# Optimization experiments

Measured on AMD Instinct MI355X. Metric: run time of the kernel, lower is better.

The kernel has to match this reference:

```python
import jax, jax.numpy as jnp
import numpy as np


def setup_inputs() -> dict:
    key = jax.random.key(0)
    ks = jax.random.split(key, 10)
    B, S, D = 16, 2048, 256
    return {
        "x": jax.random.normal(ks[0], (B, S, D), dtype=jnp.float32),
        "noise": jax.random.normal(ks[1], (B, S, D), dtype=jnp.float32),
        "alpha1": jax.random.normal(ks[2], (D,), dtype=jnp.float32),
        "alpha2": jax.random.normal(ks[3], (D,), dtype=jnp.float32),
        "W_ttt": jax.random.normal(ks[4], (D, D), dtype=jnp.float32),
        "W_proj": jax.random.normal(ks[5], (D, D), dtype=jnp.float32),
        "ff_alpha": jax.random.normal(ks[6], (D,), dtype=jnp.float32),
        "ff_beta": jax.random.normal(ks[7], (D,), dtype=jnp.float32),
        "ff_gamma": jax.random.normal(ks[8], (1,), dtype=jnp.float32),
        "ff_eta": jax.random.normal(ks[9], (1,), dtype=jnp.float32),
    }


def _ttt(W, m, noise):
    # m, noise: [B, S, D]; sequential SGD on W over the sequence axis.
    B, S, D = m.shape
    scale = 2.0 / (B * D)  # d(mse)/d(pred) factor

    def step(W, inp):
        state, eps = inp                      # [B, D] each
        train = state + eps
        diff = train @ W.T - state            # pred - label, [B, D]
        grad = scale * (diff.T @ train)       # dL/dW, [D, D]
        Wn = W - 0.01 * grad
        return Wn, state @ Wn.T               # readout with updated W

    _, outs = jax.lax.scan(step, W, (jnp.swapaxes(m, 0, 1), jnp.swapaxes(noise, 0, 1)))
    return jnp.swapaxes(outs, 0, 1)           # [B, S, D]


def reference(x, noise, alpha1, alpha2, W_ttt, W_proj, ff_alpha, ff_beta, ff_gamma, ff_eta):
    # memory path: VecDyT norm then TTT (readouts are detached in torch)
    m = jnp.tanh(alpha1 * x)
    mem = jax.lax.stop_gradient(_ttt(W_ttt, m, noise))

    # feedforward path: VecDyT norm then FFUnit
    v = jnp.tanh(alpha2 * x)
    u = ff_gamma * jax.nn.gelu(ff_alpha * v, approximate=False) + ff_eta * jnp.sin(ff_beta * v)
    g = u * (v @ W_proj.T)

    return mem + g
```

## Files before the change

kernel.cpp:

```cpp
#include <hip/hip_runtime.h>

typedef unsigned short u16;
typedef unsigned int u32;
typedef __attribute__((ext_vector_type(8))) short bf16x8;
typedef __attribute__((ext_vector_type(4))) float f32x4;

#define SB 16
#define SS 2048
#define SD 256
#define CC 16
#define NCH (SS / CC)
#define KAPPA 4.8828125e-6f
#define RP 24
#define SLOT 65536

__device__ __forceinline__ u16 f2bf(float f) {
  u32 u = __float_as_uint(f);
  u = (u + 0x7FFFu + ((u >> 16) & 1u)) >> 16;
  return (u16)u;
}
__device__ __forceinline__ float bf2f(u16 u) { return __uint_as_float((u32)u << 16); }

__device__ __forceinline__ bf16x8 ldfrag(const u16* p) {
  union { uint4 u; bf16x8 f; } cv;
  cv.u = *(const uint4*)p;
  return cv.f;
}
__device__ __forceinline__ bf16x8 asfrag(uint4 q) {
  union { uint4 u; bf16x8 f; } cv;
  cv.u = q;
  return cv.f;
}
__device__ __forceinline__ f32x4 mfma16(bf16x8 a, bf16x8 b, f32x4 c) {
  return __builtin_amdgcn_mfma_f32_16x16x32_bf16(a, b, c, 0, 0, 0);
}

__global__ __launch_bounds__(256) void prep_kernel(
    const float* __restrict__ x, const float* __restrict__ noise,
    const float* __restrict__ a1,
    u16* __restrict__ train, u16* __restrict__ state, u16* __restrict__ trainT) {
  size_t i4 = (size_t)blockIdx.x * 256 + threadIdx.x;
  size_t base = i4 * 4;
  int d = (int)(base & 255);
  int t = (int)((base >> 8) & 2047);
  int b = (int)(base >> 19);
  float4 xv = *(const float4*)(x + base);
  float4 nv = *(const float4*)(noise + base);
  float4 av = *(const float4*)(a1 + d);
  float m0 = tanhf(av.x * xv.x);
  float m1 = tanhf(av.y * xv.y);
  float m2 = tanhf(av.z * xv.z);
  float m3 = tanhf(av.w * xv.w);
  size_t dst = ((size_t)t * SB + b) * SD + d;
  ushort4 tr, st;
  tr.x = f2bf(m0 + nv.x); tr.y = f2bf(m1 + nv.y);
  tr.z = f2bf(m2 + nv.z); tr.w = f2bf(m3 + nv.w);
  st.x = f2bf(m0); st.y = f2bf(m1); st.z = f2bf(m2); st.w = f2bf(m3);
  *(ushort4*)(train + dst) = tr;
  *(ushort4*)(state + dst) = st;
  size_t tb = ((size_t)t * SD + d) * SB + b;
  trainT[tb + 0 * SB] = tr.x;
  trainT[tb + 1 * SB] = tr.y;
  trainT[tb + 2 * SB] = tr.z;
  trainT[tb + 3 * SB] = tr.w;
}

__global__ __launch_bounds__(256) void gram2ff_kernel(
    const u16* __restrict__ tr, const u16* __restrict__ st,
    u16* __restrict__ AG, u16* __restrict__ LbG,
    const float* __restrict__ x, const float* __restrict__ a2,
    const float* __restrict__ Wp, const float* __restrict__ ffa,
    const float* __restrict__ ffb, const float* __restrict__ ffg_,
    const float* __restrict__ ffe_, float* __restrict__ out) {
  __shared__ float As[32][68];
  __shared__ float Bs[32][68];
  const int tid = threadIdx.x;

  if (blockIdx.x < 2048) {
    const int cb = blockIdx.x;
    const int c = cb >> 4, t = cb & 15;
    const int lane = tid & 63, wv = tid >> 6;
    const int lr = lane & 15, lq = lane >> 4;
    const size_t Tt = (size_t)cb;
    bf16x8 trF[8], stF[8];
#pragma unroll
    for (int k = 0; k < 8; ++k) {
      trF[k] = ldfrag(tr + (Tt * 16 + lr) * 256 + k * 32 + lq * 8);
      stF[k] = ldfrag(st + (Tt * 16 + lr) * 256 + k * 32 + lq * 8);
    }
    for (int ii = 0; ii < 2; ++ii) {
      const int sp = wv + ii * 4;
      u16* dA = AG + ((size_t)cb * 8 + sp) * 512;
      u16* dL = LbG + ((size_t)cb * 8 + sp) * 512;
#pragma unroll
      for (int h = 0; h < 2; ++h) {
        const int s = 2 * sp + h;
        f32x4 accA = {0.f, 0.f, 0.f, 0.f}, accL = {0.f, 0.f, 0.f, 0.f};
        if (s <= t) {
          const u16* bsrc = tr + ((size_t)(c * 16 + s) * 16 + lr) * 256 + lq * 8;
#pragma unroll
          for (int k = 0; k < 8; ++k) {
            bf16x8 bk = ldfrag(bsrc + k * 32);
            if (s < t) accA = mfma16(trF[k], bk, accA);
            accL = mfma16(stF[k], bk, accL);
          }
        }
#pragma unroll
        for (int r = 0; r < 4; ++r) {
          int idx = (lq * 4 + r) * 32 + h * 16 + lr;
          dA[idx] = (s < t) ? f2bf(accA[r]) : (u16)0;
          dL[idx] = (s <= t) ? f2bf(accL[r]) : (u16)0;
        }
      }
    }
    return;
  }

  const int fb = blockIdx.x - 2048;
  const int gm0 = (fb >> 2) * 64;
  const int gn0 = (fb & 3) * 64;
  const int tm = tid & 15, tn = tid >> 4;
  const int lr = tid & 63;
  const int lq = tid >> 6;
  float acc[4][4];
#pragma unroll
  for (int i = 0; i < 4; i++)
#pragma unroll
    for (int j = 0; j < 4; j++) acc[i][j] = 0.f;

  for (int k0 = 0; k0 < 256; k0 += 32) {
    {
      const float* xp = x + (size_t)(gm0 + lr) * 256 + k0 + lq * 8;
      float4 v0 = *(const float4*)(xp);
      float4 v1 = *(const float4*)(xp + 4);
      const float* ap = a2 + k0 + lq * 8;
      float4 a0 = *(const float4*)(ap);
      float4 a1v = *(const float4*)(ap + 4);
      As[lq * 8 + 0][lr] = tanhf(a0.x * v0.x);
      As[lq * 8 + 1][lr] = tanhf(a0.y * v0.y);
      As[lq * 8 + 2][lr] = tanhf(a0.z * v0.z);
      As[lq * 8 + 3][lr] = tanhf(a0.w * v0.w);
      As[lq * 8 + 4][lr] = tanhf(a1v.x * v1.x);
      As[lq * 8 + 5][lr] = tanhf(a1v.y * v1.y);
      As[lq * 8 + 6][lr] = tanhf(a1v.z * v1.z);
      As[lq * 8 + 7][lr] = tanhf(a1v.w * v1.w);
      const float* wp = Wp + (size_t)(gn0 + lr) * 256 + k0 + lq * 8;
      float4 w0 = *(const float4*)(wp);
      float4 w1 = *(const float4*)(wp + 4);
      Bs[lq * 8 + 0][lr] = w0.x; Bs[lq * 8 + 1][lr] = w0.y;
      Bs[lq * 8 + 2][lr] = w0.z; Bs[lq * 8 + 3][lr] = w0.w;
      Bs[lq * 8 + 4][lr] = w1.x; Bs[lq * 8 + 5][lr] = w1.y;
      Bs[lq * 8 + 6][lr] = w1.z; Bs[lq * 8 + 7][lr] = w1.w;
    }
    __syncthreads();
#pragma unroll
    for (int k = 0; k < 32; ++k) {
      float4 av4 = *(const float4*)&As[k][tm * 4];
      float4 bv4 = *(const float4*)&Bs[k][tn * 4];
      float a[4] = {av4.x, av4.y, av4.z, av4.w};
      float b[4] = {bv4.x, bv4.y, bv4.z, bv4.w};
#pragma unroll
      for (int i = 0; i < 4; i++)
#pragma unroll
        for (int j = 0; j < 4; j++) acc[i][j] += a[i] * b[j];
    }
    __syncthreads();
  }
  const float ga = ffg_[0], et = ffe_[0];
#pragma unroll
  for (int ii = 0; ii < 4; ++ii) {
    int row = gm0 + tm * 4 + ii;
    int col = gn0 + tn * 4;
    float4 xv = *(const float4*)(x + (size_t)row * 256 + col);
    float4 fa = *(const float4*)(ffa + col);
    float4 fb4 = *(const float4*)(ffb + col);
    float4 a2v = *(const float4*)(a2 + col);
    float xs[4] = {xv.x, xv.y, xv.z, xv.w};
    float fas[4] = {fa.x, fa.y, fa.z, fa.w};
    float fbs[4] = {fb4.x, fb4.y, fb4.z, fb4.w};
    float a2s[4] = {a2v.x, a2v.y, a2v.z, a2v.w};
    float res[4];
#pragma unroll
    for (int j = 0; j < 4; ++j) {
      float v = tanhf(a2s[j] * xs[j]);
      float z = fas[j] * v;
      float gelu = 0.5f * z * (1.0f + erff(z * 0.70710678118654752f));
      float u = ga * gelu + et * sinf(fbs[j] * v);
      res[j] = u * acc[ii][j];
    }
    float4 o; o.x = res[0]; o.y = res[1]; o.z = res[2]; o.w = res[3];
    *(float4*)(out + (size_t)row * 256 + col) = o;
  }
}

__global__ __launch_bounds__(512) void phaseA_kernel(
    const u16* __restrict__ tr, const u16* __restrict__ st,
    const u16* __restrict__ trT, const u16* __restrict__ AG,
    u16* __restrict__ Dt, u16* __restrict__ Qb) {
  __shared__ u16 StT[CC][16 * RP];
  __shared__ u16 YtL[CC][16 * RP];
  __shared__ u16 ZtL[CC][16 * RP];
  const int tid = threadIdx.x;
  const int lane = tid & 63;
  const int w = tid >> 6;
  const int d1b = blockIdx.x;
  const int c = blockIdx.y;
  const int lr = lane & 15;
  const int lq = lane >> 4;

  uint4 agR[2][8];
#pragma unroll
  for (int u = 0; u < 2; ++u) {
    const u16* ag = AG + ((size_t)(c * 16 + w + 8 * u) * 8) * 512 + lr * 32 + lq * 8;
#pragma unroll
    for (int sp = 0; sp < 8; ++sp) agR[u][sp] = *(const uint4*)(ag + sp * 512);
  }
  u16 sraw[2][4];
  float xs[2][4];
#pragma unroll
  for (int u = 0; u < 2; ++u) {
    const size_t T = (size_t)c * CC + w + 8 * u;
    ushort4 pk;
#pragma unroll
    for (int r = 0; r < 4; ++r) {
      size_t idx = (T * 16 + lq * 4 + r) * 256 + d1b * 16 + lr;
      sraw[u][r] = st[idx];
      xs[u][r] = bf2f(tr[idx]);
      ((u16*)&pk)[r] = sraw[u][r];
    }
    *(ushort4*)(&StT[w + 8 * u][lr * RP + lq * 4]) = pk;
  }
  __syncthreads();

#pragma unroll
  for (int u = 0; u < 2; ++u) {
    f32x4 a1 = {0.f, 0.f, 0.f, 0.f}, a2 = {0.f, 0.f, 0.f, 0.f};
#pragma unroll
    for (int sp = 0; sp < 8; ++sp) {
      const int s0 = 2 * sp + (lq >> 1);
      bf16x8 xb = ldfrag(trT + ((size_t)(c * CC + s0) * 256 + d1b * 16 + lr) * 16 +
                         (lq & 1) * 8);
      bf16x8 sb = ldfrag(&StT[s0][lr * RP + (lq & 1) * 8]);
      a1 = mfma16(asfrag(agR[u][sp]), xb, a1);
      a2 = mfma16(asfrag(agR[u][sp]), sb, a2);
    }
    ushort4 py, pz;
#pragma unroll
    for (int r = 0; r < 4; ++r) {
      ((u16*)&py)[r] = f2bf(xs[u][r] - KAPPA * a1[r]);
      ((u16*)&pz)[r] = f2bf(bf2f(sraw[u][r]) - KAPPA * a2[r]);
    }
    *(ushort4*)(&YtL[w + 8 * u][lr * RP + lq * 4]) = py;
    *(ushort4*)(&ZtL[w + 8 * u][lr * RP + lq * 4]) = pz;
  }
  __syncthreads();

  bf16x8 yf[8], zf[8];
#pragma unroll
  for (int sp = 0; sp < 8; ++sp) {
    yf[sp] = ldfrag(&YtL[2 * sp + (lq >> 1)][lr * RP + (lq & 1) * 8]);
    zf[sp] = ldfrag(&ZtL[2 * sp + (lq >> 1)][lr * RP + (lq & 1) * 8]);
  }
  const size_t base = (size_t)c * SLOT;
#pragma unroll
  for (int u = 0; u < 2; ++u) {
    const int d2b = w + 8 * u;
    f32x4 da = {0.f, 0.f, 0.f, 0.f}, qa = {0.f, 0.f, 0.f, 0.f};
#pragma unroll
    for (int sp = 0; sp < 8; ++sp) {
      bf16x8 xb = ldfrag(trT + ((size_t)(c * CC + 2 * sp + (lq >> 1)) * 256 +
                                d2b * 16 + lr) * 16 + (lq & 1) * 8);
      da = mfma16(yf[sp], xb, da);
      qa = mfma16(zf[sp], xb, qa);
    }
#pragma unroll
    for (int r = 0; r < 4; ++r) {
      Dt[base + (size_t)(d2b * 16 + lr) * 256 + d1b * 16 + lq * 4 + r] =
          f2bf(-KAPPA * da[r]);
      Qb[base + (size_t)(d1b * 16 + lq * 4 + r) * 256 + d2b * 16 + lr] =
          f2bf(KAPPA * qa[r]);
    }
  }
}

__global__ __launch_bounds__(512) void kq_kernel(
    const u16* __restrict__ Dt, u16* __restrict__ Qb, int lev) {
  const int qn = blockIdx.x >> 4, rb = blockIdx.x & 15;
  const int half = 1 << (lev - 1);
  const int blk = qn >> (lev - 1), win = qn & (half - 1);
  const int i = blk * half * 2 + half + win;
  const int j = blk * half * 2 + half - 1;
  u16* Qi = Qb + (size_t)i * SLOT;
  const u16* Qj = Qb + (size_t)j * SLOT;
  const u16* Dti = Dt + (size_t)i * SLOT;
  const int lane = threadIdx.x & 63, w = threadIdx.x >> 6;
  const int lr = lane & 15, lq = lane >> 4;
  bf16x8 aq[8];
#pragma unroll
  for (int kb = 0; kb < 8; ++kb)
    aq[kb] = ldfrag(Qj + (size_t)(rb * 16 + lr) * 256 + kb * 32 + lq * 8);
#pragma unroll
  for (int u = 0; u < 2; ++u) {
    const int cb = w + 8 * u;
    f32x4 acc = {0.f, 0.f, 0.f, 0.f};
#pragma unroll
    for (int kb = 0; kb < 8; ++kb) {
      bf16x8 bf = ldfrag(Dti + (size_t)(cb * 16 + lr) * 256 + kb * 32 + lq * 8);
      acc = mfma16(aq[kb], bf, acc);
    }
#pragma unroll
    for (int r = 0; r < 4; ++r) {
      size_t idx = (size_t)(rb * 16 + lq * 4 + r) * 256 + cb * 16 + lr;
      float v = acc[r] + bf2f(Qj[idx]) + bf2f(Qi[idx]);
      Qi[idx] = f2bf(v);
    }
  }
}

__global__ __launch_bounds__(512) void kd_kernel(u16* __restrict__ Dt, int lev) {
  const int qn = blockIdx.x >> 4, rb = blockIdx.x & 15;
  const int half = 1 << (lev - 1);
  const int blk = qn >> (lev - 1), win = qn & (half - 1);
  const int i = blk * half * 2 + half + win;
  const int j = blk * half * 2 + half - 1;
  u16* Dti = Dt + (size_t)i * SLOT;
  const u16* Dtj = Dt + (size_t)j * SLOT;
  const int lane = threadIdx.x & 63, w = threadIdx.x >> 6;
  const int lr = lane & 15, lq = lane >> 4;
  bf16x8 ad[8];
#pragma unroll
  for (int kb = 0; kb < 8; ++kb)
    ad[kb] = ldfrag(Dti + (size_t)(rb * 16 + lr) * 256 + kb * 32 + lq * 8);
  float oldv[2][4];
#pragma unroll
  for (int u = 0; u < 2; ++u) {
    const int cb = w + 8 * u;
#pragma unroll
    for (int r = 0; r < 4; ++r) {
      size_t idx = (size_t)(rb * 16 + lq * 4 + r) * 256 + cb * 16 + lr;
      oldv[u][r] = bf2f(Dtj[idx]) + bf2f(Dti[idx]);
    }
  }
  __syncthreads();
#pragma unroll
  for (int u = 0; u < 2; ++u) {
    const int cb = w + 8 * u;
    f32x4 acc = {0.f, 0.f, 0.f, 0.f};
#pragma unroll
    for (int kb = 0; kb < 8; ++kb) {
      union { u16 s[8]; bf16x8 f; } bv;
#pragma unroll
      for (int e = 0; e < 8; ++e)
        bv.s[e] = Dtj[(size_t)(kb * 32 + lq * 8 + e) * 256 + cb * 16 + lr];
      acc = mfma16(ad[kb], bv.f, acc);
    }
#pragma unroll
    for (int r = 0; r < 4; ++r) {
      size_t idx = (size_t)(rb * 16 + lq * 4 + r) * 256 + cb * 16 + lr;
      Dti[idx] = f2bf(acc[r] + oldv[u][r]);
    }
  }
}

__global__ __launch_bounds__(512) void phaseC_kernel(
    const u16* __restrict__ tr, const u16* __restrict__ st,
    const u16* __restrict__ AG, const u16* __restrict__ LbG,
    const u16* __restrict__ Dt, const u16* __restrict__ Qb,
    const float* __restrict__ Wttt, float* __restrict__ out) {
  __shared__ u16 RpL[CC][16 * RP];
  __shared__ u16 DpL[CC][16 * RP];
  __shared__ u16 WbL[16][268];

  const int tid = threadIdx.x;
  const int lane = tid & 63;
  const int w = tid >> 6;
  const int d1b = blockIdx.x;
  const int c = blockIdx.y;
  const int lr = lane & 15;
  const int lq = lane >> 4;

  {
    bf16x8 wf[8];
#pragma unroll
    for (int kb = 0; kb < 8; ++kb) {
      const float* wp = Wttt + (size_t)(d1b * 16 + lr) * 256 + kb * 32 + lq * 8;
      float4 w0 = *(const float4*)(wp);
      float4 w1 = *(const float4*)(wp + 4);
      union { u16 s[8]; bf16x8 f; } cv;
      cv.s[0] = f2bf(w0.x); cv.s[1] = f2bf(w0.y);
      cv.s[2] = f2bf(w0.z); cv.s[3] = f2bf(w0.w);
      cv.s[4] = f2bf(w1.x); cv.s[5] = f2bf(w1.y);
      cv.s[6] = f2bf(w1.z); cv.s[7] = f2bf(w1.w);
      wf[kb] = cv.f;
    }
    const size_t ex = (size_t)(c - 1) * SLOT;
#pragma unroll
    for (int u = 0; u < 2; ++u) {
      const int cb = w + 8 * u;
      f32x4 acc = {0.f, 0.f, 0.f, 0.f};
      if (c > 0) {
#pragma unroll
        for (int kb = 0; kb < 8; ++kb) {
          bf16x8 bf = ldfrag(Dt + ex + (size_t)(cb * 16 + lr) * 256 + kb * 32 + lq * 8);
          acc = mfma16(wf[kb], bf, acc);
        }
      }
#pragma unroll
      for (int r = 0; r < 4; ++r) {
        size_t ri = (size_t)(d1b * 16 + lq * 4 + r) * 256 + cb * 16 + lr;
        float v = Wttt[ri] + acc[r];
        if (c > 0) v += bf2f(Qb[ex + (size_t)(d1b * 16 + lq * 4 + r) * 256 + cb * 16 + lr]);
        WbL[lq * 4 + r][cb * 16 + lr] = f2bf(v);
      }
    }
  }
  __syncthreads();

  uint4 agR[2][8];
#pragma unroll
  for (int u = 0; u < 2; ++u) {
    const u16* ag = AG + ((size_t)(c * 16 + w + 8 * u) * 8) * 512 + lr * 32 + lq * 8;
#pragma unroll
    for (int sp = 0; sp < 8; ++sp) agR[u][sp] = *(const uint4*)(ag + sp * 512);
  }
  uint4 trR[2][8], stR[2][8];
  float sub[2][4];
#pragma unroll
  for (int u = 0; u < 2; ++u) {
    const size_t T = (size_t)c * CC + w + 8 * u;
    const u16* trt = tr + (T * 16 + lr) * 256 + lq * 8;
    const u16* stt = st + (T * 16 + lr) * 256 + lq * 8;
#pragma unroll
    for (int k = 0; k < 8; ++k) {
      trR[u][k] = *(const uint4*)(trt + k * 32);
      stR[u][k] = *(const uint4*)(stt + k * 32);
    }
#pragma unroll
    for (int r = 0; r < 4; ++r)
      sub[u][r] = bf2f(st[(T * 16 + lq * 4 + r) * 256 + d1b * 16 + lr]);
  }

  f32x4 rhsF[2], qF[2];
#pragma unroll
  for (int u = 0; u < 2; ++u) {
    f32x4 racc = {0.f, 0.f, 0.f, 0.f}, qacc = {0.f, 0.f, 0.f, 0.f};
#pragma unroll
    for (int k = 0; k < 8; ++k) {
      bf16x8 wb = ldfrag(&WbL[lr][k * 32 + lq * 8]);
      racc = mfma16(asfrag(trR[u][k]), wb, racc);
      qacc = mfma16(asfrag(stR[u][k]), wb, qacc);
    }
#pragma unroll
    for (int r = 0; r < 4; ++r) racc[r] -= sub[u][r];
    rhsF[u] = racc; qF[u] = qacc;
    ushort4 pk;
    pk.x = f2bf(racc.x); pk.y = f2bf(racc.y);
    pk.z = f2bf(racc.z); pk.w = f2bf(racc.w);
    *(ushort4*)(&RpL[w + 8 * u][lr * RP + lq * 4]) = pk;
  }
  __syncthreads();

  uint4 lbR[2][8];
#pragma unroll
  for (int u = 0; u < 2; ++u) {
    const u16* lb = LbG + ((size_t)(c * 16 + w + 8 * u) * 8) * 512 + lr * 32 + lq * 8;
#pragma unroll
    for (int sp = 0; sp < 8; ++sp) lbR[u][sp] = *(const uint4*)(lb + sp * 512);
  }

#pragma unroll
  for (int u = 0; u < 2; ++u) {
    f32x4 acc = {0.f, 0.f, 0.f, 0.f};
#pragma unroll
    for (int sp = 0; sp < 8; ++sp) {
      bf16x8 bf = ldfrag(&RpL[2 * sp + (lq >> 1)][lr * RP + (lq & 1) * 8]);
      acc = mfma16(asfrag(agR[u][sp]), bf, acc);
    }
    ushort4 pk;
#pragma unroll
    for (int r = 0; r < 4; ++r) {
      float dv = rhsF[u][r] - KAPPA * acc[r];
      ((u16*)&pk)[r] = f2bf(-KAPPA * dv);
    }
    *(ushort4*)(&DpL[w + 8 * u][lr * RP + lq * 4]) = pk;
  }
  __syncthreads();

  float gp[2][4];
#pragma unroll
  for (int u = 0; u < 2; ++u) {
    const size_t T = (size_t)c * CC + w + 8 * u;
#pragma unroll
    for (int r = 0; r < 4; ++r)
      gp[u][r] = out[((size_t)(lq * 4 + r) * SS + T) * SD + d1b * 16 + lr];
  }
#pragma unroll
  for (int u = 0; u < 2; ++u) {
    const size_t T = (size_t)c * CC + w + 8 * u;
    f32x4 acc = qF[u];
#pragma unroll
    for (int sp = 0; sp < 8; ++sp) {
      bf16x8 bf = ldfrag(&DpL[2 * sp + (lq >> 1)][lr * RP + (lq & 1) * 8]);
      acc = mfma16(asfrag(lbR[u][sp]), bf, acc);
    }
#pragma unroll
    for (int r = 0; r < 4; ++r) {
      size_t oi = ((size_t)(lq * 4 + r) * SS + T) * SD + d1b * 16 + lr;
      out[oi] = acc[r] + gp[u][r];
    }
  }
}

extern "C" void kernel_launch(void* const* d_in, const int* in_sizes, int n_in,
                              void* d_out, int out_size, void* d_ws, size_t ws_size,
                              hipStream_t stream) {
  const float* x     = (const float*)d_in[0];
  const float* noise = (const float*)d_in[1];
  const float* a1    = (const float*)d_in[2];
  const float* a2    = (const float*)d_in[3];
  const float* Wttt  = (const float*)d_in[4];
  const float* Wproj = (const float*)d_in[5];
  const float* ffa   = (const float*)d_in[6];
  const float* ffb   = (const float*)d_in[7];
  const float* ffg   = (const float*)d_in[8];
  const float* ffe   = (const float*)d_in[9];
  float* out = (float*)d_out;

  const size_t N = (size_t)SB * SS * SD;
  u16* tr  = (u16*)d_ws;
  u16* st  = tr + N;
  u16* trT = st + N;
  u16* AG  = trT + N;
  u16* LbG = AG + N;
  u16* Dt  = LbG + N;
  u16* Qb  = Dt + N;

  prep_kernel<<<8192, 256, 0, stream>>>(x, noise, a1, tr, st, trT);
  gram2ff_kernel<<<4096, 256, 0, stream>>>(tr, st, AG, LbG,
                                           x, a2, Wproj, ffa, ffb, ffg, ffe, out);
  phaseA_kernel<<<dim3(16, 128), 512, 0, stream>>>(tr, st, trT, AG, Dt, Qb);
  for (int lev = 1; lev <= 7; ++lev) {
    kq_kernel<<<1024, 512, 0, stream>>>(Dt, Qb, lev);
    kd_kernel<<<1024, 512, 0, stream>>>(Dt, lev);
  }
  phaseC_kernel<<<dim3(16, 128), 512, 0, stream>>>(tr, st, AG, LbG, Dt, Qb,
                                                   Wttt, out);
}
```

Baseline: 873.8 us.

## Mirror D in transposed layout and precompute per-chunk start weights

Keeps a second copy of the D matrices (Db) in the transposed layout, so the kd scan kernel can load its B operand with vectorized fragment loads instead of strided scalar gathers. The scan kernel now writes both layouts. Per-chunk starting weights W+W·D+Q are computed once per chunk in a new wstart kernel and stored in bf16 in a reused trT buffer, so the 16 phaseC blocks per chunk no longer each redo that GEMM. The cost is extra global writes for the mirror and for the Wsb buffer, plus one more kernel launch.

```diff
diff --git a/kernel.cpp b/kernel.cpp
--- a/kernel.cpp
+++ b/kernel.cpp
@@ -196,7 +196,7 @@
 __global__ __launch_bounds__(512) void phaseA_kernel(
     const u16* __restrict__ tr, const u16* __restrict__ st,
     const u16* __restrict__ trT, const u16* __restrict__ AG,
-    u16* __restrict__ Dt, u16* __restrict__ Qb) {
+    u16* __restrict__ Dt, u16* __restrict__ Db, u16* __restrict__ Qb) {
   __shared__ u16 StT[CC][16 * RP];
   __shared__ u16 YtL[CC][16 * RP];
   __shared__ u16 ZtL[CC][16 * RP];
@@ -273,13 +273,16 @@
       da = mfma16(yf[sp], xb, da);
       qa = mfma16(zf[sp], xb, qa);
     }
-#pragma unroll
-    for (int r = 0; r < 4; ++r) {
-      Dt[base + (size_t)(d2b * 16 + lr) * 256 + d1b * 16 + lq * 4 + r] =
-          f2bf(-KAPPA * da[r]);
+    ushort4 dpk;
+#pragma unroll
+    for (int r = 0; r < 4; ++r) {
+      const u16 dv = f2bf(-KAPPA * da[r]);
+      ((u16*)&dpk)[r] = dv;
+      Db[base + (size_t)(d1b * 16 + lq * 4 + r) * 256 + d2b * 16 + lr] = dv;
       Qb[base + (size_t)(d1b * 16 + lq * 4 + r) * 256 + d2b * 16 + lr] =
           f2bf(KAPPA * qa[r]);
     }
+    *(ushort4*)(Dt + base + (size_t)(d2b * 16 + lr) * 256 + d1b * 16 + lq * 4) = dpk;
   }
 }
 
@@ -317,7 +320,8 @@
   }
 }
 
-__global__ __launch_bounds__(512) void kd_kernel(u16* __restrict__ Dt, int lev) {
+__global__ __launch_bounds__(512) void kdt_kernel(
+    u16* __restrict__ Dt, u16* __restrict__ Db, int lev) {
   const int qn = blockIdx.x >> 4, rb = blockIdx.x & 15;
   const int half = 1 << (lev - 1);
   const int blk = qn >> (lev - 1), win = qn & (half - 1);
@@ -325,6 +329,8 @@
   const int j = blk * half * 2 + half - 1;
   u16* Dti = Dt + (size_t)i * SLOT;
   const u16* Dtj = Dt + (size_t)j * SLOT;
+  u16* Dbi = Db + (size_t)i * SLOT;
+  const u16* Dbj = Db + (size_t)j * SLOT;
   const int lane = threadIdx.x & 63, w = threadIdx.x >> 6;
   const int lr = lane & 15, lq = lane >> 4;
   bf16x8 ad[8];
@@ -348,42 +354,45 @@
     f32x4 acc = {0.f, 0.f, 0.f, 0.f};
 #pragma unroll
     for (int kb = 0; kb < 8; ++kb) {
-      union { u16 s[8]; bf16x8 f; } bv;
-#pragma unroll
-      for (int e = 0; e < 8; ++e)
-        bv.s[e] = Dtj[(size_t)(kb * 32 + lq * 8 + e) * 256 + cb * 16 + lr];
-      acc = mfma16(ad[kb], bv.f, acc);
-    }
-#pragma unroll
-    for (int r = 0; r < 4; ++r) {
-      size_t idx = (size_t)(rb * 16 + lq * 4 + r) * 256 + cb * 16 + lr;
-      Dti[idx] = f2bf(acc[r] + oldv[u][r]);
-    }
-  }
-}
-
-__global__ __launch_bounds__(512) void phaseC_kernel(
-    const u16* __restrict__ tr, const u16* __restrict__ st,
-    const u16* __restrict__ AG, const u16* __restrict__ LbG,
-    const u16* __restrict__ Dt, const u16* __restrict__ Qb,
-    const float* __restrict__ Wttt, float* __restrict__ out) {
-  __shared__ u16 RpL[CC][16 * RP];
-  __shared__ u16 DpL[CC][16 * RP];
-  __shared__ u16 WbL[16][268];
-
+      bf16x8 bf = ldfrag(Dbj + (size_t)(cb * 16 + lr) * 256 + kb * 32 + lq * 8);
+      acc = mfma16(ad[kb], bf, acc);
+    }
+    ushort4 mir;
+#pragma unroll
+    for (int r = 0; r < 4; ++r) {
+      const u16 nv = f2bf(acc[r] + oldv[u][r]);
+      ((u16*)&mir)[r] = nv;
+      Dti[(size_t)(rb * 16 + lq * 4 + r) * 256 + cb * 16 + lr] = nv;
+    }
+    *(ushort4*)(Dbi + (size_t)(cb * 16 + lr) * 256 + rb * 16 + lq * 4) = mir;
+  }
+}
+
+__global__ __launch_bounds__(512) void wstart_kernel(
+    const float* __restrict__ Wttt, const u16* __restrict__ Dt,
+    const u16* __restrict__ Qb, u16* __restrict__ Wsb) {
+  const int c = blockIdx.x;
   const int tid = threadIdx.x;
-  const int lane = tid & 63;
-  const int w = tid >> 6;
-  const int d1b = blockIdx.x;
-  const int c = blockIdx.y;
-  const int lr = lane & 15;
-  const int lq = lane >> 4;
-
-  {
+  const int lane = tid & 63, w = tid >> 6;
+  const int lr = lane & 15, lq = lane >> 4;
+  if (c == 0) {
+    for (int i = tid; i < SLOT / 4; i += 512) {
+      float4 v = *(const float4*)(Wttt + (size_t)i * 4);
+      ushort4 o;
+      o.x = f2bf(v.x); o.y = f2bf(v.y); o.z = f2bf(v.z); o.w = f2bf(v.w);
+      *(ushort4*)(Wsb + (size_t)i * 4) = o;
+    }
+    return;
+  }
+  const size_t ex = (size_t)(c - 1) * SLOT;
+  u16* Wc = Wsb + (size_t)c * SLOT;
+#pragma unroll
+  for (int ui = 0; ui < 2; ++ui) {
+    const int rb = w + 8 * ui;
     bf16x8 wf[8];
 #pragma unroll
     for (int kb = 0; kb < 8; ++kb) {
-      const float* wp = Wttt + (size_t)(d1b * 16 + lr) * 256 + kb * 32 + lq * 8;
+      const float* wp = Wttt + (size_t)(rb * 16 + lr) * 256 + kb * 32 + lq * 8;
       float4 w0 = *(const float4*)(wp);
       float4 w1 = *(const float4*)(wp + 4);
       union { u16 s[8]; bf16x8 f; } cv;
@@ -393,26 +402,43 @@
       cv.s[6] = f2bf(w1.z); cv.s[7] = f2bf(w1.w);
       wf[kb] = cv.f;
     }
-    const size_t ex = (size_t)(c - 1) * SLOT;
-#pragma unroll
-    for (int u = 0; u < 2; ++u) {
-      const int cb = w + 8 * u;
+    for (int cb = 0; cb < 16; ++cb) {
       f32x4 acc = {0.f, 0.f, 0.f, 0.f};
-      if (c > 0) {
-#pragma unroll
-        for (int kb = 0; kb < 8; ++kb) {
-          bf16x8 bf = ldfrag(Dt + ex + (size_t)(cb * 16 + lr) * 256 + kb * 32 + lq * 8);
-          acc = mfma16(wf[kb], bf, acc);
-        }
+#pragma unroll
+      for (int kb = 0; kb < 8; ++kb) {
+        bf16x8 bf = ldfrag(Dt + ex + (size_t)(cb * 16 + lr) * 256 + kb * 32 + lq * 8);
+        acc = mfma16(wf[kb], bf, acc);
       }
 #pragma unroll
       for (int r = 0; r < 4; ++r) {
-        size_t ri = (size_t)(d1b * 16 + lq * 4 + r) * 256 + cb * 16 + lr;
-        float v = Wttt[ri] + acc[r];
-        if (c > 0) v += bf2f(Qb[ex + (size_t)(d1b * 16 + lq * 4 + r) * 256 + cb * 16 + lr]);
-        WbL[lq * 4 + r][cb * 16 + lr] = f2bf(v);
+        size_t idx = (size_t)(rb * 16 + lq * 4 + r) * 256 + cb * 16 + lr;
+        float v = Wttt[idx] + acc[r] + bf2f(Qb[ex + idx]);
+        Wc[idx] = f2bf(v);
       }
     }
+  }
+}
+
+__global__ __launch_bounds__(512) void phaseC_kernel(
+    const u16* __restrict__ tr, const u16* __restrict__ st,
+    const u16* __restrict__ AG, const u16* __restrict__ LbG,
+    const u16* __restrict__ Wsb, float* __restrict__ out) {
+  __shared__ u16 RpL[CC][16 * RP];
+  __shared__ u16 DpL[CC][16 * RP];
+  __shared__ u16 WbL[16][268];
+
+  const int tid = threadIdx.x;
+  const int lane = tid & 63;
+  const int w = tid >> 6;
+  const int d1b = blockIdx.x;
+  const int c = blockIdx.y;
+  const int lr = lane & 15;
+  const int lq = lane >> 4;
+
+  {
+    const int row = tid >> 5, col = (tid & 31) * 8;
+    *(uint4*)&WbL[row][col] =
+        *(const uint4*)(Wsb + (size_t)c * SLOT + (size_t)(d1b * 16 + row) * 256 + col);
   }
   __syncthreads();
 
@@ -534,15 +560,17 @@
   u16* LbG = AG + N;
   u16* Dt  = LbG + N;
   u16* Qb  = Dt + N;
+  u16* Db  = Qb + N;
+  u16* Wsb = trT;
 
   prep_kernel<<<8192, 256, 0, stream>>>(x, noise, a1, tr, st, trT);
   gram2ff_kernel<<<4096, 256, 0, stream>>>(tr, st, AG, LbG,
                                            x, a2, Wproj, ffa, ffb, ffg, ffe, out);
-  phaseA_kernel<<<dim3(16, 128), 512, 0, stream>>>(tr, st, trT, AG, Dt, Qb);
+  phaseA_kernel<<<dim3(16, 128), 512, 0, stream>>>(tr, st, trT, AG, Dt, Db, Qb);
   for (int lev = 1; lev <= 7; ++lev) {
     kq_kernel<<<1024, 512, 0, stream>>>(Dt, Qb, lev);
-    kd_kernel<<<1024, 512, 0, stream>>>(Dt, lev);
-  }
-  phaseC_kernel<<<dim3(16, 128), 512, 0, stream>>>(tr, st, AG, LbG, Dt, Qb,
-                                                   Wttt, out);
-}
+    kdt_kernel<<<1024, 512, 0, stream>>>(Dt, Db, lev);
+  }
+  wstart_kernel<<<128, 512, 0, stream>>>(Wttt, Dt, Qb, Wsb);
+  phaseC_kernel<<<dim3(16, 128), 512, 0, stream>>>(tr, st, AG, LbG, Wsb, out);
+}
```

Result: slower. 919.5 us (+5.2%).
